# Kernel tuning notes

Hardware: AMD Instinct MI355X
Metric: run time of the kernel (lower is better)

## Reference

```python
import jax, jax.numpy as jnp
import numpy as np

B, L, D, H, HID = 2048, 512, 17, 8, 256  # batch, max entities, feat dim, heads, mlp hidden
SPECIAL, OUT = 9, 23  # special vector dims, policy logits (7+16)


def _lin(k, out_d, in_d, scale):
    kw, kb = jax.random.split(k)
    W = jax.random.normal(kw, (out_d, in_d), jnp.float32) * scale
    b = jax.random.normal(kb, (out_d,), jnp.float32) * 0.01
    return W, b


def setup_inputs() -> dict:
    key = jax.random.key(0)
    ks = jax.random.split(key, 16)
    # observations: row 0 holds the 9-dim special vector, rows 1..L are ragged entities
    x = jax.random.normal(ks[0], (B, L + 1, D), jnp.float32)
    lengths = jax.random.randint(ks[1], (B,), 1, L + 1)
    mask = (jnp.arange(L)[None, :] < lengths[:, None]).astype(jnp.float32)
    x = x.at[:, 1:, :].multiply(mask[:, :, None])  # zero rows mark padding
    s = 1.0 / np.sqrt(D)
    # per-head K/V projections (num_heads separate tiny Linears)
    Wk = jax.random.normal(ks[2], (H, D, D), jnp.float32) * s
    bk = jax.random.normal(ks[3], (H, D), jnp.float32) * 0.01
    Wv = jax.random.normal(ks[4], (H, D, D), jnp.float32) * s
    bv = jax.random.normal(ks[5], (H, D), jnp.float32) * 0.01
    q = jax.random.normal(ks[6], (H, D), jnp.float32)  # learned per-head queries
    Wo, bo = _lin(ks[7], D, H * D, 1.0 / np.sqrt(H * D))
    sc = 1.0 / np.sqrt(D + SPECIAL)
    pW1, pb1 = _lin(ks[8], HID, D + SPECIAL, sc)
    pW2, pb2 = _lin(ks[9], HID, HID, 1.0 / np.sqrt(HID))
    pW3, pb3 = _lin(ks[10], OUT, HID, 1.0 / np.sqrt(HID))
    vW1, vb1 = _lin(ks[11], HID, D + SPECIAL, sc)
    vW2, vb2 = _lin(ks[12], HID, HID, 1.0 / np.sqrt(HID))
    vW3, vb3 = _lin(ks[13], 1, HID, 1.0 / np.sqrt(HID))
    return dict(x=x, Wk=Wk, bk=bk, Wv=Wv, bv=bv, q=q, Wo=Wo, bo=bo,
                pW1=pW1, pb1=pb1, pW2=pW2, pb2=pb2, pW3=pW3, pb3=pb3,
                vW1=vW1, vb1=vb1, vW2=vW2, vb2=vb2, vW3=vW3, vb3=vb3)


def _mlp(h, W1, b1, W2, b2, W3, b3):
    h = jax.nn.relu(h @ W1.T + b1)
    h = jax.nn.relu(h @ W2.T + b2)
    return h @ W3.T + b3


def reference(x, Wk, bk, Wv, bv, q, Wo, bo,
              pW1, pb1, pW2, pb2, pW3, pb3,
              vW1, vb1, vW2, vb2, vW3, vb3):
    special = x[:, 0, :SPECIAL]            # [B, 9]
    seq = x[:, 1:, :]                      # [B, L, D]
    mask = jnp.sum(jnp.abs(seq), axis=-1) != 0  # [B, L] non-padded rows
    # per-head keys/values for all samples at once (batched over the head loop)
    keys = jnp.einsum('bld,hed->bhle', seq, Wk) + bk[None, :, None, :]   # [B,H,L,D]
    vals = jnp.einsum('bld,hed->bhle', seq, Wv) + bv[None, :, None, :]   # [B,H,L,D]
    scores = jnp.einsum('bhle,he->bhl', keys, q)                          # [B,H,L]
    scores = jnp.where(mask[:, None, :], scores, -1e9)
    w = jax.nn.softmax(scores, axis=-1)                                   # [B,H,L]
    agg = jnp.einsum('bhl,bhle->bhe', w, vals).reshape(x.shape[0], H * D)  # concat heads
    attn = agg @ Wo.T + bo                                                # [B, D]
    comb = jnp.concatenate([attn, special], axis=-1)                      # [B, D+9]
    logits = _mlp(comb, pW1, pb1, pW2, pb2, pW3, pb3)                     # [B, 23]
    value = _mlp(comb, vW1, vb1, vW2, vb2, vW3, vb3)                      # [B, 1]
    return logits, value
```

## Files before the change

kernel.cpp:

```cpp
#include <hip/hip_runtime.h>
#include <hip/hip_bf16.h>

#define B_ 2048
#define D_ 17
#define H_ 8
#define HID_ 256
#define OUT_ 23
#define XROW 8721

__device__ __forceinline__ float4 ld4u(const float* p) {
  float4 v; __builtin_memcpy(&v, p, 16); return v;
}
__device__ __forceinline__ float bclane(float v, int l) {
  return __uint_as_float(__builtin_amdgcn_readlane(__float_as_uint(v), l));
}

__global__ __launch_bounds__(256) void prep_kernel(
    const float* __restrict__ pW2, const float* __restrict__ vW2,
    const float* __restrict__ Wk, const float* __restrict__ bk,
    const float* __restrict__ q,
    float* __restrict__ pW2t, float* __restrict__ vW2t, float* __restrict__ qkc)
{
  const int bid = blockIdx.x;
  const int t = threadIdx.x;
  if (bid == 128) {
    if (t < H_ * D_) {
      const int h = t / D_, dd = t - h * D_;
      float s = 0.f;
      #pragma unroll
      for (int e = 0; e < D_; ++e) s = fmaf(Wk[h*289 + e*D_ + dd], q[h*D_ + e], s);
      qkc[h*18 + dd] = s;
    } else if (t < H_ * D_ + H_) {
      const int h = t - H_ * D_;
      float s = 0.f;
      #pragma unroll
      for (int e = 0; e < D_; ++e) s = fmaf(bk[h*D_ + e], q[h*D_ + e], s);
      qkc[h*18 + 17] = s;
    }
    return;
  }
  __shared__ float tile[32][33];
  const int m = bid >> 6, tid = bid & 63;
  const int ti = (tid >> 3) * 32, tk = (tid & 7) * 32;
  const float* src = m ? vW2 : pW2;
  float* dst = m ? vW2t : pW2t;
  const int tx = t & 31, ty = t >> 5;
  #pragma unroll
  for (int r = 0; r < 4; ++r) tile[ty + 8*r][tx] = src[(ti + ty + 8*r)*HID_ + tk + tx];
  __syncthreads();
  #pragma unroll
  for (int r = 0; r < 4; ++r) dst[(tk + ty + 8*r)*HID_ + ti + tx] = tile[tx][ty + 8*r];
}

__global__ __launch_bounds__(256, 6) void attn_part_kernel(
    const float* __restrict__ x, const float* __restrict__ qkc,
    float* __restrict__ part)
{
  const int b = blockIdx.x;
  const int t = threadIdx.x;
  const int w = t >> 6, lane = t & 63;
  const int h = lane & 7, rg = lane >> 3;
  const float* xs = x + (size_t)b * XROW + D_;

  float qk[D_];
  #pragma unroll
  for (int d = 0; d < D_; ++d) qk[d] = qkc[h*18 + d];
  const float chr = qkc[h*18 + 17];

  float den = 0.f, acc[D_];
  #pragma unroll
  for (int d = 0; d < D_; ++d) acc[d] = 0.f;

  const float* rb = xs + (size_t)rg * D_;
  float4 A0, A1, A2, A3; float A4;
  float4 C0, C1, C2, C3; float C4;
  auto loadA = [&](int c) {
    const float* rp = rb + c * 136;
    A0 = ld4u(rp); A1 = ld4u(rp+4); A2 = ld4u(rp+8); A3 = ld4u(rp+12); A4 = rp[16];
  };
  auto loadC = [&](int c) {
    const float* rp = rb + c * 136;
    C0 = ld4u(rp); C1 = ld4u(rp+4); C2 = ld4u(rp+8); C3 = ld4u(rp+12); C4 = rp[16];
  };
  auto comp = [&](const float4& v0, const float4& v1, const float4& v2, const float4& v3, float v4) {
    float sc = chr;
    sc = fmaf(qk[0],  v0.x, sc); sc = fmaf(qk[1],  v0.y, sc);
    sc = fmaf(qk[2],  v0.z, sc); sc = fmaf(qk[3],  v0.w, sc);
    sc = fmaf(qk[4],  v1.x, sc); sc = fmaf(qk[5],  v1.y, sc);
    sc = fmaf(qk[6],  v1.z, sc); sc = fmaf(qk[7],  v1.w, sc);
    sc = fmaf(qk[8],  v2.x, sc); sc = fmaf(qk[9],  v2.y, sc);
    sc = fmaf(qk[10], v2.z, sc); sc = fmaf(qk[11], v2.w, sc);
    sc = fmaf(qk[12], v3.x, sc); sc = fmaf(qk[13], v3.y, sc);
    sc = fmaf(qk[14], v3.z, sc); sc = fmaf(qk[15], v3.w, sc);
    sc = fmaf(qk[16], v4, sc);
    const float p = (v0.x != 0.f) ? __expf(sc) : 0.f;
    den += p;
    acc[0]  = fmaf(p, v0.x, acc[0]);  acc[1]  = fmaf(p, v0.y, acc[1]);
    acc[2]  = fmaf(p, v0.z, acc[2]);  acc[3]  = fmaf(p, v0.w, acc[3]);
    acc[4]  = fmaf(p, v1.x, acc[4]);  acc[5]  = fmaf(p, v1.y, acc[5]);
    acc[6]  = fmaf(p, v1.z, acc[6]);  acc[7]  = fmaf(p, v1.w, acc[7]);
    acc[8]  = fmaf(p, v2.x, acc[8]);  acc[9]  = fmaf(p, v2.y, acc[9]);
    acc[10] = fmaf(p, v2.z, acc[10]); acc[11] = fmaf(p, v2.w, acc[11]);
    acc[12] = fmaf(p, v3.x, acc[12]); acc[13] = fmaf(p, v3.y, acc[13]);
    acc[14] = fmaf(p, v3.z, acc[14]); acc[15] = fmaf(p, v3.w, acc[15]);
    acc[16] = fmaf(p, v4, acc[16]);
  };

  loadA(w);
  #pragma unroll 1
  for (int c = w; c < 64; c += 8) {
    if (c + 4 < 64) loadC(c + 4);
    if (__ballot(A0.x != 0.f) == 0ull) break;
    comp(A0, A1, A2, A3, A4);
    if (c + 4 >= 64) break;
    if (c + 8 < 64) loadA(c + 8);
    if (__ballot(C0.x != 0.f) == 0ull) break;
    comp(C0, C1, C2, C3, C4);
  }

  #pragma unroll
  for (int m = 8; m <= 32; m <<= 1) {
    den += __shfl_xor(den, m, 64);
    #pragma unroll
    for (int d = 0; d < D_; ++d) acc[d] += __shfl_xor(acc[d], m, 64);
  }
  if (lane < 8) {
    float* pp = part + ((size_t)b * 4 + w) * 144 + lane * 18;
    pp[0] = den;
    #pragma unroll
    for (int d = 0; d < D_; ++d) pp[1 + d] = acc[d];
  }
}

__global__ __launch_bounds__(512) void mlp_fused_kernel(
    const float* __restrict__ x, const float* __restrict__ part,
    const float* __restrict__ Wv, const float* __restrict__ bv,
    const float* __restrict__ Wo, const float* __restrict__ bo,
    const float* __restrict__ pW1, const float* __restrict__ pb1,
    const float* __restrict__ pW2t, const float* __restrict__ pb2,
    const float* __restrict__ pW3, const float* __restrict__ pb3,
    const float* __restrict__ vW1, const float* __restrict__ vb1,
    const float* __restrict__ vW2t, const float* __restrict__ vb2,
    const float* __restrict__ vW3, const float* __restrict__ vb3,
    float* __restrict__ out)
{
  __shared__ float s_swn[8][136];
  __shared__ float s_agg[8][136];
  __shared__ float s_wp[8][136];
  __shared__ float s_comb[8][26];
  __shared__ __align__(16) float s_red[2][3][8][HID_];
  __shared__ __align__(16) float s_h2[2][8][HID_];

  const int t = threadIdx.x;
  const int b0 = blockIdx.x * 8;
  const int cb = t >> 6;
  const int cl = t & 63;

  {
    const float* pb_ = part + (size_t)(b0 + cb) * 4 * 144;
    for (int u = cl; u < 136; u += 64) {
      const int hh = u / D_, d = u - hh * D_;
      const float dn = pb_[hh*18] + pb_[144 + hh*18] + pb_[288 + hh*18] + pb_[432 + hh*18];
      const float ac = pb_[hh*18+1+d] + pb_[144 + hh*18+1+d] + pb_[288 + hh*18+1+d] + pb_[432 + hh*18+1+d];
      s_swn[cb][u] = ac / dn;
    }
  }
  __syncthreads();
  for (int u = cl; u < 136; u += 64) {
    const int hh = u / D_, e = u - hh * D_;
    float s = bv[u];
    #pragma unroll
    for (int d = 0; d < D_; ++d) s = fmaf(Wv[hh*289 + e*D_ + d], s_swn[cb][hh*D_ + d], s);
    s_agg[cb][u] = s;
  }
  __syncthreads();
  for (int u = cl; u < 136; u += 64) {
    const int o = u >> 3, pt = u & 7;
    float s = 0.f;
    #pragma unroll
    for (int j = 0; j < D_; ++j) s = fmaf(Wo[o*136 + pt*D_ + j], s_agg[cb][pt*D_ + j], s);
    s_wp[cb][u] = s;
  }
  __syncthreads();
  if (cl < D_) {
    float s = bo[cl];
    #pragma unroll
    for (int pt = 0; pt < 8; ++pt) s += s_wp[cb][cl*8 + pt];
    s_comb[cb][cl] = s;
  } else if (cl < 26) {
    s_comb[cb][cl] = x[(size_t)(b0 + cb) * XROW + (cl - D_)];
  }
  __syncthreads();

  const int p = t >> 8;
  const int kq = (t >> 6) & 3;
  const int ln = t & 63;
  const float* W1  = p ? vW1  : pW1;   const float* B1 = p ? vb1 : pb1;
  const float* W2t = p ? vW2t : pW2t;  const float* B2 = p ? vb2 : pb2;

  float h[8];
  {
    const int i = kq * 64 + ln;
    float a[8];
    #pragma unroll
    for (int bb = 0; bb < 8; ++bb) a[bb] = 0.f;
    const float* wr = W1 + i * 26;
    for (int k = 0; k < 26; ++k) {
      const float wk = wr[k];
      #pragma unroll
      for (int bb = 0; bb < 8; ++bb) a[bb] = fmaf(wk, s_comb[bb][k], a[bb]);
    }
    const float bias = B1[i];
    #pragma unroll
    for (int bb = 0; bb < 8; ++bb) h[bb] = fmaxf(a[bb] + bias, 0.f);
  }

  float4 acc[8];
  #pragma unroll
  for (int bb = 0; bb < 8; ++bb) acc[bb] = make_float4(0.f, 0.f, 0.f, 0.f);
  {
    const float* wbase = W2t + (size_t)(kq * 64) * HID_ + 4 * ln;
    #pragma unroll 8
    for (int jj = 0; jj < 64; ++jj) {
      const float4 wv = *(const float4*)(wbase + (size_t)jj * HID_);
      #pragma unroll
      for (int bb = 0; bb < 8; ++bb) {
        const float hv = bclane(h[bb], jj);
        acc[bb].x = fmaf(wv.x, hv, acc[bb].x);
        acc[bb].y = fmaf(wv.y, hv, acc[bb].y);
        acc[bb].z = fmaf(wv.z, hv, acc[bb].z);
        acc[bb].w = fmaf(wv.w, hv, acc[bb].w);
      }
    }
  }
  if (kq > 0) {
    #pragma unroll
    for (int bb = 0; bb < 8; ++bb) *(float4*)&s_red[p][kq - 1][bb][4 * ln] = acc[bb];
  }
  __syncthreads();
  if (kq == 0) {
    const float4 bias = *(const float4*)&B2[4 * ln];
    #pragma unroll
    for (int bb = 0; bb < 8; ++bb) {
      const float4 r0 = *(const float4*)&s_red[p][0][bb][4 * ln];
      const float4 r1 = *(const float4*)&s_red[p][1][bb][4 * ln];
      const float4 r2 = *(const float4*)&s_red[p][2][bb][4 * ln];
      float4 r;
      r.x = fmaxf(acc[bb].x + r0.x + r1.x + r2.x + bias.x, 0.f);
      r.y = fmaxf(acc[bb].y + r0.y + r1.y + r2.y + bias.y, 0.f);
      r.z = fmaxf(acc[bb].z + r0.z + r1.z + r2.z + bias.z, 0.f);
      r.w = fmaxf(acc[bb].w + r0.w + r1.w + r2.w + bias.w, 0.f);
      *(float4*)&s_h2[p][bb][4 * ln] = r;
    }
  }
  __syncthreads();

  if (t < 184) {
    const int bb = t / OUT_, o = t - bb * OUT_;
    const float4* w4 = (const float4*)(pW3 + o * HID_);
    const float4* h4 = (const float4*)&s_h2[0][bb][0];
    float s = pb3[o];
    for (int k = 0; k < 64; ++k) {
      const float4 wv = w4[k], hv = h4[k];
      s = fmaf(wv.x, hv.x, fmaf(wv.y, hv.y, fmaf(wv.z, hv.z, fmaf(wv.w, hv.w, s))));
    }
    out[(size_t)(b0 + bb) * OUT_ + o] = s;
  } else if (t >= 256 && t < 264) {
    const int bb = t - 256;
    const float4* w4 = (const float4*)vW3;
    const float4* h4 = (const float4*)&s_h2[1][bb][0];
    float s = vb3[0];
    for (int k = 0; k < 64; ++k) {
      const float4 wv = w4[k], hv = h4[k];
      s = fmaf(wv.x, hv.x, fmaf(wv.y, hv.y, fmaf(wv.z, hv.z, fmaf(wv.w, hv.w, s))));
    }
    out[(size_t)B_ * OUT_ + b0 + bb] = s;
  }
}

extern "C" void kernel_launch(void* const* d_in, const int* in_sizes, int n_in,
                              void* d_out, int out_size, void* d_ws, size_t ws_size,
                              hipStream_t stream) {
  (void)in_sizes; (void)n_in; (void)out_size; (void)ws_size;
  const float* x   = (const float*)d_in[0];
  const float* Wk  = (const float*)d_in[1];
  const float* bk  = (const float*)d_in[2];
  const float* Wv  = (const float*)d_in[3];
  const float* bv  = (const float*)d_in[4];
  const float* q   = (const float*)d_in[5];
  const float* Wo  = (const float*)d_in[6];
  const float* bo  = (const float*)d_in[7];
  const float* pW1 = (const float*)d_in[8];
  const float* pb1 = (const float*)d_in[9];
  const float* pW2 = (const float*)d_in[10];
  const float* pb2 = (const float*)d_in[11];
  const float* pW3 = (const float*)d_in[12];
  const float* pb3 = (const float*)d_in[13];
  const float* vW1 = (const float*)d_in[14];
  const float* vb1 = (const float*)d_in[15];
  const float* vW2 = (const float*)d_in[16];
  const float* vb2 = (const float*)d_in[17];
  const float* vW3 = (const float*)d_in[18];
  const float* vb3 = (const float*)d_in[19];
  float* out = (float*)d_out;

  float* pW2t = (float*)d_ws;
  float* vW2t = pW2t + (size_t)HID_ * HID_;
  float* qkc  = vW2t + (size_t)HID_ * HID_;
  float* part = qkc + 160;

  prep_kernel<<<129, 256, 0, stream>>>(pW2, vW2, Wk, bk, q, pW2t, vW2t, qkc);
  attn_part_kernel<<<B_, 256, 0, stream>>>(x, qkc, part);
  mlp_fused_kernel<<<B_ / 8, 512, 0, stream>>>(x, part, Wv, bv, Wo, bo,
                                               pW1, pb1, pW2t, pb2, pW3, pb3,
                                               vW1, vb1, vW2t, vb2, vW3, vb3, out);
}
```

Baseline: 64.71 us.

## Remap attention work so each lane handles two heads over 16 rows

Reorganises the attention partial kernel. Each wave now covers half of one sample's sequence, and each lane computes two heads over rows strided by 16, so every loaded row feeds two heads instead of one. Each block processes two samples, and there are two partials per sample instead of four, which cuts redundant global loads of x by half. In exchange, register pressure rises (two accumulators of 17 floats each plus two row buffers), occupancy drops from 6 to 4 blocks, and early exit is coarser because it is decided per half-sequence wave.

```diff
diff --git a/kernel.cpp b/kernel.cpp
--- a/kernel.cpp
+++ b/kernel.cpp
@@ -52,83 +52,93 @@
   for (int r = 0; r < 4; ++r) dst[(tk + ty + 8*r)*HID_ + ti + tx] = tile[tx][ty + 8*r];
 }
 
-__global__ __launch_bounds__(256, 6) void attn_part_kernel(
+__global__ __launch_bounds__(256, 4) void attn_part_kernel(
     const float* __restrict__ x, const float* __restrict__ qkc,
     float* __restrict__ part)
 {
-  const int b = blockIdx.x;
   const int t = threadIdx.x;
   const int w = t >> 6, lane = t & 63;
-  const int h = lane & 7, rg = lane >> 3;
-  const float* xs = x + (size_t)b * XROW + D_;
-
-  float qk[D_];
-  #pragma unroll
-  for (int d = 0; d < D_; ++d) qk[d] = qkc[h*18 + d];
-  const float chr = qkc[h*18 + 17];
-
-  float den = 0.f, acc[D_];
-  #pragma unroll
-  for (int d = 0; d < D_; ++d) acc[d] = 0.f;
-
-  const float* rb = xs + (size_t)rg * D_;
-  float4 A0, A1, A2, A3; float A4;
-  float4 C0, C1, C2, C3; float C4;
-  auto loadA = [&](int c) {
-    const float* rp = rb + c * 136;
-    A0 = ld4u(rp); A1 = ld4u(rp+4); A2 = ld4u(rp+8); A3 = ld4u(rp+12); A4 = rp[16];
+  const int hp = lane >> 4;
+  const int r  = lane & 15;
+  const int b    = blockIdx.x * 2 + (w >> 1);
+  const int half = w & 1;
+
+  const float* xs = x + (size_t)b * XROW + D_ + (size_t)(half << 8) * D_;
+  const float* rb = xs + (size_t)r * D_;
+
+  const float* q0 = qkc + (2*hp) * 18;
+  const float* q1 = q0 + 18;
+  float qk0[D_], qk1[D_];
+  #pragma unroll
+  for (int d = 0; d < D_; ++d) { qk0[d] = q0[d]; qk1[d] = q1[d]; }
+  const float ch0 = q0[17], ch1 = q1[17];
+
+  float den0 = 0.f, den1 = 0.f;
+  float acc0[D_], acc1[D_];
+  #pragma unroll
+  for (int d = 0; d < D_; ++d) { acc0[d] = 0.f; acc1[d] = 0.f; }
+
+  float A[D_], C[D_];
+  auto loadA = [&](int ph) {
+    const float* rp = rb + ph * 272;
+    const float4 v0 = ld4u(rp), v1 = ld4u(rp+4), v2 = ld4u(rp+8), v3 = ld4u(rp+12);
+    A[0]=v0.x; A[1]=v0.y; A[2]=v0.z; A[3]=v0.w;
+    A[4]=v1.x; A[5]=v1.y; A[6]=v1.z; A[7]=v1.w;
+    A[8]=v2.x; A[9]=v2.y; A[10]=v2.z; A[11]=v2.w;
+    A[12]=v3.x; A[13]=v3.y; A[14]=v3.z; A[15]=v3.w;
+    A[16]=rp[16];
   };
-  auto loadC = [&](int c) {
-    const float* rp = rb + c * 136;
-    C0 = ld4u(rp); C1 = ld4u(rp+4); C2 = ld4u(rp+8); C3 = ld4u(rp+12); C4 = rp[16];
+  auto loadC = [&](int ph) {
+    const float* rp = rb + ph * 272;
+    const float4 v0 = ld4u(rp), v1 = ld4u(rp+4), v2 = ld4u(rp+8), v3 = ld4u(rp+12);
+    C[0]=v0.x; C[1]=v0.y; C[2]=v0.z; C[3]=v0.w;
+    C[4]=v1.x; C[5]=v1.y; C[6]=v1.z; C[7]=v1.w;
+    C[8]=v2.x; C[9]=v2.y; C[10]=v2.z; C[11]=v2.w;
+    C[12]=v3.x; C[13]=v3.y; C[14]=v3.z; C[15]=v3.w;
+    C[16]=rp[16];
   };
-  auto comp = [&](const float4& v0, const float4& v1, const float4& v2, const float4& v3, float v4) {
-    float sc = chr;
-    sc = fmaf(qk[0],  v0.x, sc); sc = fmaf(qk[1],  v0.y, sc);
-    sc = fmaf(qk[2],  v0.z, sc); sc = fmaf(qk[3],  v0.w, sc);
-    sc = fmaf(qk[4],  v1.x, sc); sc = fmaf(qk[5],  v1.y, sc);
-    sc = fmaf(qk[6],  v1.z, sc); sc = fmaf(qk[7],  v1.w, sc);
-    sc = fmaf(qk[8],  v2.x, sc); sc = fmaf(qk[9],  v2.y, sc);
-    sc = fmaf(qk[10], v2.z, sc); sc = fmaf(qk[11], v2.w, sc);
-    sc = fmaf(qk[12], v3.x, sc); sc = fmaf(qk[13], v3.y, sc);
-    sc = fmaf(qk[14], v3.z, sc); sc = fmaf(qk[15], v3.w, sc);
-    sc = fmaf(qk[16], v4, sc);
-    const float p = (v0.x != 0.f) ? __expf(sc) : 0.f;
-    den += p;
-    acc[0]  = fmaf(p, v0.x, acc[0]);  acc[1]  = fmaf(p, v0.y, acc[1]);
-    acc[2]  = fmaf(p, v0.z, acc[2]);  acc[3]  = fmaf(p, v0.w, acc[3]);
-    acc[4]  = fmaf(p, v1.x, acc[4]);  acc[5]  = fmaf(p, v1.y, acc[5]);
-    acc[6]  = fmaf(p, v1.z, acc[6]);  acc[7]  = fmaf(p, v1.w, acc[7]);
-    acc[8]  = fmaf(p, v2.x, acc[8]);  acc[9]  = fmaf(p, v2.y, acc[9]);
-    acc[10] = fmaf(p, v2.z, acc[10]); acc[11] = fmaf(p, v2.w, acc[11]);
-    acc[12] = fmaf(p, v3.x, acc[12]); acc[13] = fmaf(p, v3.y, acc[13]);
-    acc[14] = fmaf(p, v3.z, acc[14]); acc[15] = fmaf(p, v3.w, acc[15]);
-    acc[16] = fmaf(p, v4, acc[16]);
+  auto comp = [&](const float* f) {
+    float s0 = ch0, s1 = ch1;
+    #pragma unroll
+    for (int d = 0; d < D_; ++d) { s0 = fmaf(qk0[d], f[d], s0); s1 = fmaf(qk1[d], f[d], s1); }
+    const bool live = (f[0] != 0.f);
+    const float p0 = live ? __expf(s0) : 0.f;
+    const float p1 = live ? __expf(s1) : 0.f;
+    den0 += p0; den1 += p1;
+    #pragma unroll
+    for (int d = 0; d < D_; ++d) {
+      acc0[d] = fmaf(p0, f[d], acc0[d]);
+      acc1[d] = fmaf(p1, f[d], acc1[d]);
+    }
   };
 
-  loadA(w);
+  loadA(0);
   #pragma unroll 1
-  for (int c = w; c < 64; c += 8) {
-    if (c + 4 < 64) loadC(c + 4);
-    if (__ballot(A0.x != 0.f) == 0ull) break;
-    comp(A0, A1, A2, A3, A4);
-    if (c + 4 >= 64) break;
-    if (c + 8 < 64) loadA(c + 8);
-    if (__ballot(C0.x != 0.f) == 0ull) break;
-    comp(C0, C1, C2, C3, C4);
-  }
-
-  #pragma unroll
-  for (int m = 8; m <= 32; m <<= 1) {
-    den += __shfl_xor(den, m, 64);
-    #pragma unroll
-    for (int d = 0; d < D_; ++d) acc[d] += __shfl_xor(acc[d], m, 64);
-  }
-  if (lane < 8) {
-    float* pp = part + ((size_t)b * 4 + w) * 144 + lane * 18;
-    pp[0] = den;
-    #pragma unroll
-    for (int d = 0; d < D_; ++d) pp[1 + d] = acc[d];
+  for (int ph = 0; ph < 16; ph += 2) {
+    if (ph + 1 < 16) loadC(ph + 1);
+    if (__ballot(A[0] != 0.f) == 0ull) break;
+    comp(A);
+    if (ph + 1 >= 16) break;
+    if (ph + 2 < 16) loadA(ph + 2);
+    if (__ballot(C[0] != 0.f) == 0ull) break;
+    comp(C);
+  }
+
+  #pragma unroll
+  for (int m = 1; m <= 8; m <<= 1) {
+    den0 += __shfl_xor(den0, m, 64);
+    den1 += __shfl_xor(den1, m, 64);
+    #pragma unroll
+    for (int d = 0; d < D_; ++d) {
+      acc0[d] += __shfl_xor(acc0[d], m, 64);
+      acc1[d] += __shfl_xor(acc1[d], m, 64);
+    }
+  }
+  if (r == 0) {
+    float* pp = part + ((size_t)b * 2 + half) * 144 + (2*hp) * 18;
+    pp[0] = den0; pp[18] = den1;
+    #pragma unroll
+    for (int d = 0; d < D_; ++d) { pp[1 + d] = acc0[d]; pp[19 + d] = acc1[d]; }
   }
 }
 
@@ -157,11 +167,11 @@
   const int cl = t & 63;
 
   {
-    const float* pb_ = part + (size_t)(b0 + cb) * 4 * 144;
+    const float* pb_ = part + (size_t)(b0 + cb) * 288;
     for (int u = cl; u < 136; u += 64) {
       const int hh = u / D_, d = u - hh * D_;
-      const float dn = pb_[hh*18] + pb_[144 + hh*18] + pb_[288 + hh*18] + pb_[432 + hh*18];
-      const float ac = pb_[hh*18+1+d] + pb_[144 + hh*18+1+d] + pb_[288 + hh*18+1+d] + pb_[432 + hh*18+1+d];
+      const float dn = pb_[hh*18] + pb_[144 + hh*18];
+      const float ac = pb_[hh*18 + 1 + d] + pb_[144 + hh*18 + 1 + d];
       s_swn[cb][u] = ac / dn;
     }
   }
@@ -245,12 +255,12 @@
       const float4 r0 = *(const float4*)&s_red[p][0][bb][4 * ln];
       const float4 r1 = *(const float4*)&s_red[p][1][bb][4 * ln];
       const float4 r2 = *(const float4*)&s_red[p][2][bb][4 * ln];
-      float4 r;
-      r.x = fmaxf(acc[bb].x + r0.x + r1.x + r2.x + bias.x, 0.f);
-      r.y = fmaxf(acc[bb].y + r0.y + r1.y + r2.y + bias.y, 0.f);
-      r.z = fmaxf(acc[bb].z + r0.z + r1.z + r2.z + bias.z, 0.f);
-      r.w = fmaxf(acc[bb].w + r0.w + r1.w + r2.w + bias.w, 0.f);
-      *(float4*)&s_h2[p][bb][4 * ln] = r;
+      float4 rr;
+      rr.x = fmaxf(acc[bb].x + r0.x + r1.x + r2.x + bias.x, 0.f);
+      rr.y = fmaxf(acc[bb].y + r0.y + r1.y + r2.y + bias.y, 0.f);
+      rr.z = fmaxf(acc[bb].z + r0.z + r1.z + r2.z + bias.z, 0.f);
+      rr.w = fmaxf(acc[bb].w + r0.w + r1.w + r2.w + bias.w, 0.f);
+      *(float4*)&s_h2[p][bb][4 * ln] = rr;
     }
   }
   __syncthreads();
@@ -310,7 +320,7 @@
   float* part = qkc + 160;
 
   prep_kernel<<<129, 256, 0, stream>>>(pW2, vW2, Wk, bk, q, pW2t, vW2t, qkc);
-  attn_part_kernel<<<B_, 256, 0, stream>>>(x, qkc, part);
+  attn_part_kernel<<<B_ / 2, 256, 0, stream>>>(x, qkc, part);
   mlp_fused_kernel<<<B_ / 8, 512, 0, stream>>>(x, part, Wv, bv, Wo, bo,
                                                pW1, pb1, pW2t, pb2, pW3, pb3,
                                                vW1, vb1, vW2t, vb2, vW3, vb3, out);
```

Result: no change. 63.52 us (-1.8%).

## Move head reduction and Wv/Wo projection into attention kernel epilogue

Applied to the files above, without the earlier changes.

Moves the cross-wave reduction of partial softmax sums and the Wv/Wo projections out of the MLP kernel into the end of the attention kernel, using shared memory. Only the 26-float combined vector per sample goes to global memory instead of four 144-float partials. The MLP kernel now just loads the combined vectors. The attention kernel's occupancy hint goes from 6 to 8 blocks per CU, which may force register spilling and adds a serial projection tail to each block.

```diff
diff --git a/kernel.cpp b/kernel.cpp
--- a/kernel.cpp
+++ b/kernel.cpp
@@ -52,12 +52,19 @@
   for (int r = 0; r < 4; ++r) dst[(tk + ty + 8*r)*HID_ + ti + tx] = tile[tx][ty + 8*r];
 }
 
-__global__ __launch_bounds__(256, 6) void attn_part_kernel(
+__global__ __launch_bounds__(256, 8) void attn_comb_kernel(
     const float* __restrict__ x, const float* __restrict__ qkc,
-    float* __restrict__ part)
+    const float* __restrict__ Wv, const float* __restrict__ bv,
+    const float* __restrict__ Wo, const float* __restrict__ bo,
+    float* __restrict__ comb)
 {
+  __shared__ float s_part[4][H_][18];
+  __shared__ float s_swn[136];
+  __shared__ float s_agg[136];
+  __shared__ float s_wp[136];
+
+  const int t = threadIdx.x;
   const int b = blockIdx.x;
-  const int t = threadIdx.x;
   const int w = t >> 6, lane = t & 63;
   const int h = lane & 7, rg = lane >> 3;
   const float* xs = x + (size_t)b * XROW + D_;
@@ -125,17 +132,49 @@
     for (int d = 0; d < D_; ++d) acc[d] += __shfl_xor(acc[d], m, 64);
   }
   if (lane < 8) {
-    float* pp = part + ((size_t)b * 4 + w) * 144 + lane * 18;
+    float* pp = &s_part[w][lane][0];
     pp[0] = den;
     #pragma unroll
     for (int d = 0; d < D_; ++d) pp[1 + d] = acc[d];
   }
-}
-
-__global__ __launch_bounds__(512) void mlp_fused_kernel(
-    const float* __restrict__ x, const float* __restrict__ part,
-    const float* __restrict__ Wv, const float* __restrict__ bv,
-    const float* __restrict__ Wo, const float* __restrict__ bo,
+  __syncthreads();
+
+  if (t < 136) {
+    const int hh = t / D_, d = t - hh * D_;
+    float dn = 0.f, ac = 0.f;
+    #pragma unroll
+    for (int ww = 0; ww < 4; ++ww) { dn += s_part[ww][hh][0]; ac += s_part[ww][hh][1 + d]; }
+    s_swn[t] = ac / dn;
+  }
+  __syncthreads();
+  if (t < 136) {
+    const int hh = t / D_, e = t - hh * D_;
+    float s = bv[t];
+    #pragma unroll
+    for (int d = 0; d < D_; ++d) s = fmaf(Wv[hh*289 + e*D_ + d], s_swn[hh*D_ + d], s);
+    s_agg[t] = s;
+  }
+  __syncthreads();
+  if (t < 136) {
+    const int o = t >> 3, pt = t & 7;
+    float s = 0.f;
+    #pragma unroll
+    for (int j = 0; j < D_; ++j) s = fmaf(Wo[o*136 + pt*D_ + j], s_agg[pt*D_ + j], s);
+    s_wp[t] = s;
+  }
+  __syncthreads();
+  if (t < D_) {
+    float s = bo[t];
+    #pragma unroll
+    for (int pt = 0; pt < 8; ++pt) s += s_wp[t*8 + pt];
+    comb[b*26 + t] = s;
+  } else if (t < 26) {
+    comb[b*26 + t] = x[(size_t)b * XROW + (t - D_)];
+  }
+}
+
+__global__ __launch_bounds__(512) void mlp_kernel(
+    const float* __restrict__ comb,
     const float* __restrict__ pW1, const float* __restrict__ pb1,
     const float* __restrict__ pW2t, const float* __restrict__ pb2,
     const float* __restrict__ pW3, const float* __restrict__ pb3,
@@ -144,57 +183,19 @@
     const float* __restrict__ vW3, const float* __restrict__ vb3,
     float* __restrict__ out)
 {
-  __shared__ float s_swn[8][136];
-  __shared__ float s_agg[8][136];
-  __shared__ float s_wp[8][136];
   __shared__ float s_comb[8][26];
   __shared__ __align__(16) float s_red[2][3][8][HID_];
   __shared__ __align__(16) float s_h2[2][8][HID_];
 
   const int t = threadIdx.x;
   const int b0 = blockIdx.x * 8;
-  const int cb = t >> 6;
-  const int cl = t & 63;
-
-  {
-    const float* pb_ = part + (size_t)(b0 + cb) * 4 * 144;
-    for (int u = cl; u < 136; u += 64) {
-      const int hh = u / D_, d = u - hh * D_;
-      const float dn = pb_[hh*18] + pb_[144 + hh*18] + pb_[288 + hh*18] + pb_[432 + hh*18];
-      const float ac = pb_[hh*18+1+d] + pb_[144 + hh*18+1+d] + pb_[288 + hh*18+1+d] + pb_[432 + hh*18+1+d];
-      s_swn[cb][u] = ac / dn;
-    }
-  }
-  __syncthreads();
-  for (int u = cl; u < 136; u += 64) {
-    const int hh = u / D_, e = u - hh * D_;
-    float s = bv[u];
-    #pragma unroll
-    for (int d = 0; d < D_; ++d) s = fmaf(Wv[hh*289 + e*D_ + d], s_swn[cb][hh*D_ + d], s);
-    s_agg[cb][u] = s;
-  }
-  __syncthreads();
-  for (int u = cl; u < 136; u += 64) {
-    const int o = u >> 3, pt = u & 7;
-    float s = 0.f;
-    #pragma unroll
-    for (int j = 0; j < D_; ++j) s = fmaf(Wo[o*136 + pt*D_ + j], s_agg[cb][pt*D_ + j], s);
-    s_wp[cb][u] = s;
-  }
-  __syncthreads();
-  if (cl < D_) {
-    float s = bo[cl];
-    #pragma unroll
-    for (int pt = 0; pt < 8; ++pt) s += s_wp[cb][cl*8 + pt];
-    s_comb[cb][cl] = s;
-  } else if (cl < 26) {
-    s_comb[cb][cl] = x[(size_t)(b0 + cb) * XROW + (cl - D_)];
-  }
-  __syncthreads();
-
   const int p = t >> 8;
   const int kq = (t >> 6) & 3;
   const int ln = t & 63;
+
+  if (t < 208) { const int bb = t / 26, k = t - bb*26; s_comb[bb][k] = comb[(size_t)(b0 + bb)*26 + k]; }
+  __syncthreads();
+
   const float* W1  = p ? vW1  : pW1;   const float* B1 = p ? vb1 : pb1;
   const float* W2t = p ? vW2t : pW2t;  const float* B2 = p ? vb2 : pb2;
 
@@ -245,12 +246,12 @@
       const float4 r0 = *(const float4*)&s_red[p][0][bb][4 * ln];
       const float4 r1 = *(const float4*)&s_red[p][1][bb][4 * ln];
       const float4 r2 = *(const float4*)&s_red[p][2][bb][4 * ln];
-      float4 r;
-      r.x = fmaxf(acc[bb].x + r0.x + r1.x + r2.x + bias.x, 0.f);
-      r.y = fmaxf(acc[bb].y + r0.y + r1.y + r2.y + bias.y, 0.f);
-      r.z = fmaxf(acc[bb].z + r0.z + r1.z + r2.z + bias.z, 0.f);
-      r.w = fmaxf(acc[bb].w + r0.w + r1.w + r2.w + bias.w, 0.f);
-      *(float4*)&s_h2[p][bb][4 * ln] = r;
+      float4 rr;
+      rr.x = fmaxf(acc[bb].x + r0.x + r1.x + r2.x + bias.x, 0.f);
+      rr.y = fmaxf(acc[bb].y + r0.y + r1.y + r2.y + bias.y, 0.f);
+      rr.z = fmaxf(acc[bb].z + r0.z + r1.z + r2.z + bias.z, 0.f);
+      rr.w = fmaxf(acc[bb].w + r0.w + r1.w + r2.w + bias.w, 0.f);
+      *(float4*)&s_h2[p][bb][4 * ln] = rr;
     }
   }
   __syncthreads();
@@ -307,11 +308,10 @@
   float* pW2t = (float*)d_ws;
   float* vW2t = pW2t + (size_t)HID_ * HID_;
   float* qkc  = vW2t + (size_t)HID_ * HID_;
-  float* part = qkc + 160;
+  float* comb = qkc + 160;
 
   prep_kernel<<<129, 256, 0, stream>>>(pW2, vW2, Wk, bk, q, pW2t, vW2t, qkc);
-  attn_part_kernel<<<B_, 256, 0, stream>>>(x, qkc, part);
-  mlp_fused_kernel<<<B_ / 8, 512, 0, stream>>>(x, part, Wv, bv, Wo, bo,
-                                               pW1, pb1, pW2t, pb2, pW3, pb3,
-                                               vW1, vb1, vW2t, vb2, vW3, vb3, out);
-}
+  attn_comb_kernel<<<B_, 256, 0, stream>>>(x, qkc, Wv, bv, Wo, bo, comb);
+  mlp_kernel<<<B_ / 8, 512, 0, stream>>>(comb, pW1, pb1, pW2t, pb2, pW3, pb3,
+                                         vW1, vb1, vW2t, vb2, vW3, vb3, out);
+}
```

Measured after the change: 141.0 us. 118% more time.
